# Optimization experiments

Measured on AMD Instinct MI355X. Metric: run time of the kernel, lower is better.

The kernel has to match this reference:

```python
import jax, jax.numpy as jnp
import numpy as np

E, IN, OUT, T, CAP = 8, 2048, 2048, 16384, 2304

def setup_inputs() -> dict:
    key = jax.random.key(0)
    k1, k2, k3 = jax.random.split(key, 3)
    x = jax.random.normal(k1, (T, IN), dtype=jnp.float32)
    # weight stored as (E, out_features, in_features), matching weight.view(-1, out, in)
    weight = jax.random.normal(k2, (E, OUT, IN), dtype=jnp.float32) / np.float32(np.sqrt(IN))
    bias = jax.random.normal(k3, (E, OUT), dtype=jnp.float32) * 0.01
    # expert-sorted ragged counts, sum == T, max == CAP
    tokens_per_expert = jnp.array([2304, 2048, 2048, 2048, 2048, 2048, 2048, 1792], dtype=jnp.int32)
    return {"x": x, "weight": weight, "bias": bias,
            "tokens_per_expert": tokens_per_expert, "capacity": CAP}

def reference(x, weight, bias, tokens_per_expert, capacity):
    # x: [T, in] expert-sorted tokens; weight: [E, out, in]; bias: [E, out]
    T_, d = x.shape
    E_ = weight.shape[0]
    # expert id per token (jit-friendly ragged repeat with static total length)
    ids = jnp.repeat(jnp.arange(E_, dtype=jnp.int32), tokens_per_expert,
                     total_repeat_length=T_)                        # [T]
    offsets = jnp.concatenate([jnp.zeros((1,), jnp.int32),
                               jnp.cumsum(tokens_per_expert)[:-1].astype(jnp.int32)])
    pos = jnp.arange(T_, dtype=jnp.int32) - offsets[ids]            # slot within expert block
    # dispatch to padded per-expert buffers, batched GEMM, gather back
    grouped = jnp.zeros((E_, capacity, d), x.dtype).at[ids, pos].set(x)   # [E, cap, in]
    yg = jnp.einsum('ecd,eod->eco', grouped, weight)                      # [E, cap, out]
    out = yg[ids, pos] + bias[ids]                                        # fused bias add
    return out
```

## Files before the change

kernel.cpp:

```cpp
#include <hip/hip_runtime.h>


typedef __attribute__((ext_vector_type(8))) short short8;
typedef __attribute__((ext_vector_type(4))) float f32x4;

__device__ __forceinline__ unsigned short f2bf(float f) {
    unsigned u = __builtin_bit_cast(unsigned, f);
    u += 0x7FFFu + ((u >> 16) & 1u);
    return (unsigned short)(u >> 16);
}

__global__ __launch_bounds__(256)
void cvt_f32_bf16(const float* __restrict__ in, unsigned short* __restrict__ out, int n8)
{
    int i = blockIdx.x * blockDim.x + threadIdx.x;
    const int stride = gridDim.x * blockDim.x;
    const f32x4* __restrict__ in4 = (const f32x4*)in;
    short8* __restrict__ out8 = (short8*)out;
    for (; i < n8; i += stride) {
        f32x4 a = in4[2 * i];
        f32x4 b = in4[2 * i + 1];
        short8 o;
        o[0] = (short)f2bf(a.x); o[1] = (short)f2bf(a.y);
        o[2] = (short)f2bf(a.z); o[3] = (short)f2bf(a.w);
        o[4] = (short)f2bf(b.x); o[5] = (short)f2bf(b.y);
        o[6] = (short)f2bf(b.z); o[7] = (short)f2bf(b.w);
        out8[i] = o;
    }
}

__device__ __forceinline__ void gload16(const unsigned short* g, unsigned short* l)
{
    __builtin_amdgcn_global_load_lds(
        (const __attribute__((address_space(1))) unsigned int*)g,
        (__attribute__((address_space(3))) unsigned int*)l, 16, 0, 0);
}

#define BARRIER() do { asm volatile("" ::: "memory"); \
    __builtin_amdgcn_s_barrier(); \
    asm volatile("" ::: "memory"); } while (0)
#define LGK0() asm volatile("s_waitcnt lgkmcnt(0)" ::: "memory")
#define VM(N)  asm volatile("s_waitcnt vmcnt(" #N ")" ::: "memory")

__global__ __launch_bounds__(512, 1)
void grouped_gemm_8ph(const unsigned short* __restrict__ xb,
                      const unsigned short* __restrict__ wb,
                      const float* __restrict__ bias,
                      const int* __restrict__ tpe,
                      float* __restrict__ out)
{
    __shared__ __align__(16) unsigned short As[2][2][8192];
    __shared__ __align__(16) unsigned short Bs[2][2][8192];

    const int e = blockIdx.z;
    int off = 0, cnt = 0;
#pragma unroll
    for (int i = 0; i < 8; ++i) { int c = tpe[i]; if (i < e) off += c; if (i == e) cnt = c; }
    const int m0 = blockIdx.y * 256;
    if (m0 >= cnt) return;
    const int rows = min(256, cnt - m0);
    const int row0 = off + m0;
    const int n0 = blockIdx.x * 256;

    const int t    = threadIdx.x;
    const int w    = t >> 6;
    const int lane = t & 63;
    const int wr   = w >> 2;
    const int wc   = w & 3;
    const int hb   = wc >> 1;
    const int fr   = lane & 15;
    const int fq   = lane >> 4;
    const int w512 = w * 512;

    const int srow  = t >> 3;
    const int scswb = ((t & 7) * 16) ^ ((srow & 7) << 4);
    const int scsw  = scswb >> 1;

    const int ar00 = min(srow,       rows - 1);
    const int ar01 = min(srow + 64,  rows - 1);
    const int ar10 = min(srow + 128, rows - 1);
    const int ar11 = min(srow + 192, rows - 1);
    const unsigned short* aP00 = xb + (size_t)(row0 + ar00) * 2048 + scsw;
    const unsigned short* aP01 = xb + (size_t)(row0 + ar01) * 2048 + scsw;
    const unsigned short* aP10 = xb + (size_t)(row0 + ar10) * 2048 + scsw;
    const unsigned short* aP11 = xb + (size_t)(row0 + ar11) * 2048 + scsw;
    const unsigned short* wbe  = wb + (size_t)e * 4194304;
    const unsigned short* bP00 = wbe + (size_t)(n0 + srow      ) * 2048 + scsw;
    const unsigned short* bP01 = wbe + (size_t)(n0 + srow +  64) * 2048 + scsw;
    const unsigned short* bP10 = wbe + (size_t)(n0 + srow + 128) * 2048 + scsw;
    const unsigned short* bP11 = wbe + (size_t)(n0 + srow + 192) * 2048 + scsw;

#define ST_A0(P, K) do { gload16(aP00 + (K), &As[P][0][w512]); gload16(aP01 + (K), &As[P][0][4096 + w512]); } while (0)
#define ST_A1(P, K) do { gload16(aP10 + (K), &As[P][1][w512]); gload16(aP11 + (K), &As[P][1][4096 + w512]); } while (0)
#define ST_B0(P, K) do { gload16(bP00 + (K), &Bs[P][0][w512]); gload16(bP01 + (K), &Bs[P][0][4096 + w512]); } while (0)
#define ST_B1(P, K) do { gload16(bP10 + (K), &Bs[P][1][w512]); gload16(bP11 + (K), &Bs[P][1][4096 + w512]); } while (0)

    const int cs0e = (((fq * 16)     ) ^ ((fr & 7) << 4)) >> 1;
    const int cs1e = (((fq * 16) + 64) ^ ((fr & 7) << 4)) >> 1;

    short8 af[4][2], bf[4][2];

#define RD_A(P, QR) do { _Pragma("unroll") for (int mi = 0; mi < 4; ++mi) { \
        const unsigned short* _ap = &As[P][wr][((QR) * 64 + mi * 16 + fr) * 64]; \
        af[mi][0] = *(const short8*)(_ap + cs0e); \
        af[mi][1] = *(const short8*)(_ap + cs1e); } } while (0)

#define RD_B(P, H2) do { _Pragma("unroll") for (int q = 0; q < 2; ++q) { \
        const unsigned short* _bp = &Bs[P][hb][((wc & 1) * 64 + ((H2) * 2 + q) * 16 + fr) * 64]; \
        bf[(H2) * 2 + q][0] = *(const short8*)(_bp + cs0e); \
        bf[(H2) * 2 + q][1] = *(const short8*)(_bp + cs1e); } } while (0)

    f32x4 acc[8][4] = {};

#define MM16(QR, QC) do { __builtin_amdgcn_s_setprio(1); \
        _Pragma("unroll") for (int ks = 0; ks < 2; ++ks) \
        _Pragma("unroll") for (int mi = 0; mi < 4; ++mi) \
        _Pragma("unroll") for (int q = 0; q < 2; ++q) \
            acc[(QR) * 4 + mi][(QC) * 2 + q] = __builtin_amdgcn_mfma_f32_16x16x32_bf16( \
                af[mi][ks], bf[(QC) * 2 + q][ks], acc[(QR) * 4 + mi][(QC) * 2 + q], 0, 0, 0); \
        __builtin_amdgcn_s_setprio(0); } while (0)

    ST_B0(0, 0); ST_B1(0, 0); ST_A0(0, 0); ST_A1(0, 0);
    ST_B0(1, 64); ST_B1(1, 64); ST_A0(1, 64);
    VM(6);
    BARRIER();

#pragma unroll 1
    for (int i = 0; i < 16; ++i) {
        const int kb = i * 128;
        const bool stg = (i < 15);
        RD_A(0, 0); RD_B(0, 0);
        ST_A1(1, kb + 64);
        BARRIER(); LGK0();
        MM16(0, 0);
        BARRIER();
        RD_B(0, 1);
        BARRIER(); LGK0();
        MM16(0, 1);
        BARRIER();
        RD_A(0, 1);
        if (stg) { ST_B0(0, kb + 128); ST_B1(0, kb + 128); }
        BARRIER(); LGK0();
        MM16(1, 1);
        BARRIER();
        if (stg) ST_A0(0, kb + 128);
        BARRIER(); LGK0();
        MM16(1, 0);
        if (stg) { VM(6); } else { VM(0); }
        BARRIER();
        RD_A(1, 0); RD_B(1, 0);
        if (stg) ST_A1(0, kb + 128);
        BARRIER(); LGK0();
        MM16(0, 0);
        BARRIER();
        RD_B(1, 1);
        BARRIER(); LGK0();
        MM16(0, 1);
        BARRIER();
        RD_A(1, 1);
        if (stg) { ST_B0(1, kb + 192); ST_B1(1, kb + 192); }
        BARRIER(); LGK0();
        MM16(1, 1);
        BARRIER();
        if (stg) ST_A0(1, kb + 192);
        BARRIER(); LGK0();
        MM16(1, 0);
        if (stg) VM(6);
        BARRIER();
    }

#pragma unroll
    for (int nj = 0; nj < 4; ++nj) {
        const int col = n0 + wc * 64 + nj * 16 + fr;
        const float bv = bias[e * 2048 + col];
#pragma unroll
        for (int mi = 0; mi < 8; ++mi) {
            const int rb = wr * 128 + mi * 16 + fq * 4;
#pragma unroll
            for (int r = 0; r < 4; ++r) {
                const int lr = rb + r;
                if (lr < rows)
                    out[(size_t)(row0 + lr) * 2048 + col] = acc[mi][nj][r] + bv;
            }
        }
    }
#undef ST_A0
#undef ST_A1
#undef ST_B0
#undef ST_B1
#undef RD_A
#undef RD_B
#undef MM16
}

#define LDT 72

__global__ __launch_bounds__(256, 2)
void grouped_gemm_f32(const float* __restrict__ x,
                      const float* __restrict__ w,
                      const float* __restrict__ bias,
                      const int* __restrict__ tpe,
                      float* __restrict__ out)
{
    __shared__ __align__(16) unsigned short As[128 * LDT];
    __shared__ __align__(16) unsigned short Bs[128 * LDT];

    const int e = blockIdx.z;
    int off = 0, cnt = 0;
#pragma unroll
    for (int i = 0; i < 8; ++i) {
        int c = tpe[i];
        if (i < e) off += c;
        if (i == e) cnt = c;
    }
    const int m0 = blockIdx.y * 128;
    if (m0 >= cnt) return;
    const int rows = min(128, cnt - m0);
    const int row0 = off + m0;
    const int n0 = blockIdx.x * 128;

    const int tid = threadIdx.x;
    const int sr = tid >> 4;
    const int sc = (tid & 15) * 4;

    const float* gA = x + (size_t)row0 * 2048 + sc;
    const float* gB = w + (size_t)e * 4194304 + (size_t)(n0 + sr) * 2048 + sc;

    int arow[8];
#pragma unroll
    for (int p = 0; p < 8; ++p) {
        int r = sr + p * 16;
        arow[p] = ((r < rows) ? r : (rows - 1)) * 2048;
    }

    const int lane = tid & 63;
    const int wid  = tid >> 6;
    const int wm   = (wid & 1) * 64;
    const int wn   = (wid >> 1) * 64;
    const int fr   = lane & 15;
    const int fq   = lane >> 4;

    f32x4 acc[4][4];
#pragma unroll
    for (int i = 0; i < 4; ++i)
#pragma unroll
        for (int j = 0; j < 4; ++j)
            acc[i][j] = (f32x4){0.f, 0.f, 0.f, 0.f};

    for (int kt = 0; kt < 32; ++kt) {
        const int kk = kt * 64;
        __syncthreads();
#pragma unroll
        for (int p = 0; p < 8; ++p) {
            f32x4 a = *(const f32x4*)(gA + arow[p] + kk);
            f32x4 b = *(const f32x4*)(gB + p * 32768 + kk);
            const int rbase = (sr + p * 16) * LDT + sc;
            As[rbase + 0] = f2bf(a.x);
            As[rbase + 1] = f2bf(a.y);
            As[rbase + 2] = f2bf(a.z);
            As[rbase + 3] = f2bf(a.w);
            Bs[rbase + 0] = f2bf(b.x);
            Bs[rbase + 1] = f2bf(b.y);
            Bs[rbase + 2] = f2bf(b.z);
            Bs[rbase + 3] = f2bf(b.w);
        }
        __syncthreads();

#pragma unroll
        for (int ks = 0; ks < 2; ++ks) {
            short8 af[4], bfr[4];
#pragma unroll
            for (int i = 0; i < 4; ++i)
                af[i] = *(const short8*)(As + (wm + i * 16 + fr) * LDT + ks * 32 + fq * 8);
#pragma unroll
            for (int j = 0; j < 4; ++j)
                bfr[j] = *(const short8*)(Bs + (wn + j * 16 + fr) * LDT + ks * 32 + fq * 8);
#pragma unroll
            for (int i = 0; i < 4; ++i)
#pragma unroll
                for (int j = 0; j < 4; ++j)
                    acc[i][j] = __builtin_amdgcn_mfma_f32_16x16x32_bf16(af[i], bfr[j], acc[i][j], 0, 0, 0);
        }
    }

#pragma unroll
    for (int j = 0; j < 4; ++j) {
        const int col = n0 + wn + j * 16 + fr;
        const float bv = bias[e * 2048 + col];
#pragma unroll
        for (int i = 0; i < 4; ++i) {
            const int rbase = wm + i * 16 + fq * 4;
#pragma unroll
            for (int r = 0; r < 4; ++r) {
                const int lr = rbase + r;
                if (lr < rows)
                    out[(size_t)(row0 + lr) * 2048 + col] = acc[i][j][r] + bv;
            }
        }
    }
}

extern "C" void kernel_launch(void* const* d_in, const int* in_sizes, int n_in,
                              void* d_out, int out_size, void* d_ws, size_t ws_size,
                              hipStream_t stream) {
    const float* x    = (const float*)d_in[0];
    const float* w    = (const float*)d_in[1];
    const float* bias = (const float*)d_in[2];
    const int*   tpe  = (const int*)d_in[3];
    float* out = (float*)d_out;

    const size_t XE = (size_t)16384 * 2048;
    const size_t WE = (size_t)8 * 2048 * 2048;
    const size_t need = (XE + WE) * sizeof(unsigned short);

    if (ws_size >= need && d_ws != nullptr) {
        unsigned short* xb = (unsigned short*)d_ws;
        unsigned short* wbuf = xb + XE;
        cvt_f32_bf16<<<2048, 256, 0, stream>>>(x, xb, (int)(XE / 8));
        cvt_f32_bf16<<<2048, 256, 0, stream>>>(w, wbuf, (int)(WE / 8));
        dim3 grid(8, 9, 8);
        grouped_gemm_8ph<<<grid, 512, 0, stream>>>(xb, wbuf, bias, tpe, out);
    } else {
        dim3 grid(16, 18, 8);
        grouped_gemm_f32<<<grid, 256, 0, stream>>>(x, w, bias, tpe, out);
    }
}
```

Baseline: 539.5 us.

## Simplify GEMM pipeline to per-tile double buffering and fuse conversion kernels

```diff
diff --git a/kernel.cpp b/kernel.cpp
--- a/kernel.cpp
+++ b/kernel.cpp
@@ -11,21 +11,32 @@
 }
 
 __global__ __launch_bounds__(256)
-void cvt_f32_bf16(const float* __restrict__ in, unsigned short* __restrict__ out, int n8)
+void cvt2_f32_bf16(const float* __restrict__ a, unsigned short* __restrict__ ao, int na8,
+                   const float* __restrict__ b, unsigned short* __restrict__ bo, int nb8)
 {
-    int i = blockIdx.x * blockDim.x + threadIdx.x;
+    const int i0 = blockIdx.x * blockDim.x + threadIdx.x;
     const int stride = gridDim.x * blockDim.x;
-    const f32x4* __restrict__ in4 = (const f32x4*)in;
-    short8* __restrict__ out8 = (short8*)out;
-    for (; i < n8; i += stride) {
-        f32x4 a = in4[2 * i];
-        f32x4 b = in4[2 * i + 1];
+    const f32x4* __restrict__ a4 = (const f32x4*)a;
+    short8* __restrict__ a8 = (short8*)ao;
+    for (int i = i0; i < na8; i += stride) {
+        f32x4 u = a4[2 * i], v = a4[2 * i + 1];
         short8 o;
-        o[0] = (short)f2bf(a.x); o[1] = (short)f2bf(a.y);
-        o[2] = (short)f2bf(a.z); o[3] = (short)f2bf(a.w);
-        o[4] = (short)f2bf(b.x); o[5] = (short)f2bf(b.y);
-        o[6] = (short)f2bf(b.z); o[7] = (short)f2bf(b.w);
-        out8[i] = o;
+        o[0] = (short)f2bf(u.x); o[1] = (short)f2bf(u.y);
+        o[2] = (short)f2bf(u.z); o[3] = (short)f2bf(u.w);
+        o[4] = (short)f2bf(v.x); o[5] = (short)f2bf(v.y);
+        o[6] = (short)f2bf(v.z); o[7] = (short)f2bf(v.w);
+        a8[i] = o;
+    }
+    const f32x4* __restrict__ b4 = (const f32x4*)b;
+    short8* __restrict__ b8 = (short8*)bo;
+    for (int i = i0; i < nb8; i += stride) {
+        f32x4 u = b4[2 * i], v = b4[2 * i + 1];
+        short8 o;
+        o[0] = (short)f2bf(u.x); o[1] = (short)f2bf(u.y);
+        o[2] = (short)f2bf(u.z); o[3] = (short)f2bf(u.w);
+        o[4] = (short)f2bf(v.x); o[5] = (short)f2bf(v.y);
+        o[6] = (short)f2bf(v.z); o[7] = (short)f2bf(v.w);
+        b8[i] = o;
     }
 }
 
@@ -39,15 +50,14 @@
 #define BARRIER() do { asm volatile("" ::: "memory"); \
     __builtin_amdgcn_s_barrier(); \
     asm volatile("" ::: "memory"); } while (0)
-#define LGK0() asm volatile("s_waitcnt lgkmcnt(0)" ::: "memory")
-#define VM(N)  asm volatile("s_waitcnt vmcnt(" #N ")" ::: "memory")
+#define VM0()  asm volatile("s_waitcnt vmcnt(0)" ::: "memory")
 
 __global__ __launch_bounds__(512, 1)
-void grouped_gemm_8ph(const unsigned short* __restrict__ xb,
-                      const unsigned short* __restrict__ wb,
-                      const float* __restrict__ bias,
-                      const int* __restrict__ tpe,
-                      float* __restrict__ out)
+void grouped_gemm_pipe(const unsigned short* __restrict__ xb,
+                       const unsigned short* __restrict__ wb,
+                       const float* __restrict__ bias,
+                       const int* __restrict__ tpe,
+                       float* __restrict__ out)
 {
     __shared__ __align__(16) unsigned short As[2][2][8192];
     __shared__ __align__(16) unsigned short Bs[2][2][8192];
@@ -90,83 +100,63 @@
     const unsigned short* bP10 = wbe + (size_t)(n0 + srow + 128) * 2048 + scsw;
     const unsigned short* bP11 = wbe + (size_t)(n0 + srow + 192) * 2048 + scsw;
 
-#define ST_A0(P, K) do { gload16(aP00 + (K), &As[P][0][w512]); gload16(aP01 + (K), &As[P][0][4096 + w512]); } while (0)
-#define ST_A1(P, K) do { gload16(aP10 + (K), &As[P][1][w512]); gload16(aP11 + (K), &As[P][1][4096 + w512]); } while (0)
-#define ST_B0(P, K) do { gload16(bP00 + (K), &Bs[P][0][w512]); gload16(bP01 + (K), &Bs[P][0][4096 + w512]); } while (0)
-#define ST_B1(P, K) do { gload16(bP10 + (K), &Bs[P][1][w512]); gload16(bP11 + (K), &Bs[P][1][4096 + w512]); } while (0)
+#define STAGE(P, K) do { \
+        gload16(bP00 + (K), &Bs[P][0][w512]); gload16(bP01 + (K), &Bs[P][0][4096 + w512]); \
+        gload16(bP10 + (K), &Bs[P][1][w512]); gload16(bP11 + (K), &Bs[P][1][4096 + w512]); \
+        gload16(aP00 + (K), &As[P][0][w512]); gload16(aP01 + (K), &As[P][0][4096 + w512]); \
+        gload16(aP10 + (K), &As[P][1][w512]); gload16(aP11 + (K), &As[P][1][4096 + w512]); } while (0)
 
     const int cs0e = (((fq * 16)     ) ^ ((fr & 7) << 4)) >> 1;
     const int cs1e = (((fq * 16) + 64) ^ ((fr & 7) << 4)) >> 1;
 
-    short8 af[4][2], bf[4][2];
-
-#define RD_A(P, QR) do { _Pragma("unroll") for (int mi = 0; mi < 4; ++mi) { \
-        const unsigned short* _ap = &As[P][wr][((QR) * 64 + mi * 16 + fr) * 64]; \
-        af[mi][0] = *(const short8*)(_ap + cs0e); \
-        af[mi][1] = *(const short8*)(_ap + cs1e); } } while (0)
-
-#define RD_B(P, H2) do { _Pragma("unroll") for (int q = 0; q < 2; ++q) { \
-        const unsigned short* _bp = &Bs[P][hb][((wc & 1) * 64 + ((H2) * 2 + q) * 16 + fr) * 64]; \
-        bf[(H2) * 2 + q][0] = *(const short8*)(_bp + cs0e); \
-        bf[(H2) * 2 + q][1] = *(const short8*)(_bp + cs1e); } } while (0)
+    short8 a0[4][2], a1[4][2], bfr[4][2];
+
+#define RD_A0(P) do { _Pragma("unroll") for (int mi = 0; mi < 4; ++mi) { \
+        const unsigned short* _ap = &As[P][wr][(mi * 16 + fr) * 64]; \
+        a0[mi][0] = *(const short8*)(_ap + cs0e); \
+        a0[mi][1] = *(const short8*)(_ap + cs1e); } } while (0)
+
+#define RD_A1(P) do { _Pragma("unroll") for (int mi = 0; mi < 4; ++mi) { \
+        const unsigned short* _ap = &As[P][wr][(64 + mi * 16 + fr) * 64]; \
+        a1[mi][0] = *(const short8*)(_ap + cs0e); \
+        a1[mi][1] = *(const short8*)(_ap + cs1e); } } while (0)
+
+#define RD_B(P) do { _Pragma("unroll") for (int nj = 0; nj < 4; ++nj) { \
+        const unsigned short* _bp = &Bs[P][hb][((wc & 1) * 64 + nj * 16 + fr) * 64]; \
+        bfr[nj][0] = *(const short8*)(_bp + cs0e); \
+        bfr[nj][1] = *(const short8*)(_bp + cs1e); } } while (0)
 
     f32x4 acc[8][4] = {};
 
-#define MM16(QR, QC) do { __builtin_amdgcn_s_setprio(1); \
+#define TILE(P, KNEXT, STG) do { \
+        RD_A0(P); RD_B(P); RD_A1(P); \
+        __builtin_amdgcn_s_setprio(1); \
         _Pragma("unroll") for (int ks = 0; ks < 2; ++ks) \
         _Pragma("unroll") for (int mi = 0; mi < 4; ++mi) \
-        _Pragma("unroll") for (int q = 0; q < 2; ++q) \
-            acc[(QR) * 4 + mi][(QC) * 2 + q] = __builtin_amdgcn_mfma_f32_16x16x32_bf16( \
-                af[mi][ks], bf[(QC) * 2 + q][ks], acc[(QR) * 4 + mi][(QC) * 2 + q], 0, 0, 0); \
-        __builtin_amdgcn_s_setprio(0); } while (0)
-
-    ST_B0(0, 0); ST_B1(0, 0); ST_A0(0, 0); ST_A1(0, 0);
-    ST_B0(1, 64); ST_B1(1, 64); ST_A0(1, 64);
-    VM(6);
+        _Pragma("unroll") for (int nj = 0; nj < 4; ++nj) \
+            acc[mi][nj] = __builtin_amdgcn_mfma_f32_16x16x32_bf16( \
+                a0[mi][ks], bfr[nj][ks], acc[mi][nj], 0, 0, 0); \
+        _Pragma("unroll") for (int ks = 0; ks < 2; ++ks) \
+        _Pragma("unroll") for (int mi = 0; mi < 4; ++mi) \
+        _Pragma("unroll") for (int nj = 0; nj < 4; ++nj) \
+            acc[4 + mi][nj] = __builtin_amdgcn_mfma_f32_16x16x32_bf16( \
+                a1[mi][ks], bfr[nj][ks], acc[4 + mi][nj], 0, 0, 0); \
+        __builtin_amdgcn_s_setprio(0); \
+        VM0(); \
+        BARRIER(); \
+        if (STG) STAGE(P, KNEXT); } while (0)
+
+    STAGE(0, 0);
+    VM0();
     BARRIER();
+    STAGE(1, 64);
 
 #pragma unroll 1
     for (int i = 0; i < 16; ++i) {
         const int kb = i * 128;
         const bool stg = (i < 15);
-        RD_A(0, 0); RD_B(0, 0);
-        ST_A1(1, kb + 64);
-        BARRIER(); LGK0();
-        MM16(0, 0);
-        BARRIER();
-        RD_B(0, 1);
-        BARRIER(); LGK0();
-        MM16(0, 1);
-        BARRIER();
-        RD_A(0, 1);
-        if (stg) { ST_B0(0, kb + 128); ST_B1(0, kb + 128); }
-        BARRIER(); LGK0();
-        MM16(1, 1);
-        BARRIER();
-        if (stg) ST_A0(0, kb + 128);
-        BARRIER(); LGK0();
-        MM16(1, 0);
-        if (stg) { VM(6); } else { VM(0); }
-        BARRIER();
-        RD_A(1, 0); RD_B(1, 0);
-        if (stg) ST_A1(0, kb + 128);
-        BARRIER(); LGK0();
-        MM16(0, 0);
-        BARRIER();
-        RD_B(1, 1);
-        BARRIER(); LGK0();
-        MM16(0, 1);
-        BARRIER();
-        RD_A(1, 1);
-        if (stg) { ST_B0(1, kb + 192); ST_B1(1, kb + 192); }
-        BARRIER(); LGK0();
-        MM16(1, 1);
-        BARRIER();
-        if (stg) ST_A0(1, kb + 192);
-        BARRIER(); LGK0();
-        MM16(1, 0);
-        if (stg) VM(6);
-        BARRIER();
+        TILE(0, kb + 128, stg);
+        TILE(1, kb + 192, stg);
     }
 
 #pragma unroll
@@ -184,13 +174,11 @@
             }
         }
     }
-#undef ST_A0
-#undef ST_A1
-#undef ST_B0
-#undef ST_B1
-#undef RD_A
+#undef STAGE
+#undef RD_A0
+#undef RD_A1
 #undef RD_B
-#undef MM16
+#undef TILE
 }
 
 #define LDT 72
@@ -316,10 +304,10 @@
     if (ws_size >= need && d_ws != nullptr) {
         unsigned short* xb = (unsigned short*)d_ws;
         unsigned short* wbuf = xb + XE;
-        cvt_f32_bf16<<<2048, 256, 0, stream>>>(x, xb, (int)(XE / 8));
-        cvt_f32_bf16<<<2048, 256, 0, stream>>>(w, wbuf, (int)(WE / 8));
+        cvt2_f32_bf16<<<2048, 256, 0, stream>>>(x, xb, (int)(XE / 8),
+                                                w, wbuf, (int)(WE / 8));
         dim3 grid(8, 9, 8);
-        grouped_gemm_8ph<<<grid, 512, 0, stream>>>(xb, wbuf, bias, tpe, out);
+        grouped_gemm_pipe<<<grid, 512, 0, stream>>>(xb, wbuf, bias, tpe, out);
     } else {
         dim3 grid(16, 18, 8);
         grouped_gemm_f32<<<grid, 256, 0, stream>>>(x, w, bias, tpe, out);
```

Result: slower. 609.4 us (+13.0%).
